# Kernel tuning notes

Measured on AMD Instinct MI355X. Metric: run time of the kernel, lower is better.

The kernel has to match this reference:

```python
import jax, jax.numpy as jnp
import numpy as np

B, S, E, H = 2, 2048, 1024, 16
D = E // H  # head_dim = 64
SCALE = 1.0 / np.sqrt(D)


def setup_inputs() -> dict:
    key = jax.random.key(0)
    ks = jax.random.split(key, 5)
    std = 0.02
    return {
        "x": jax.random.normal(ks[0], (B, S, E), dtype=jnp.float32),
        "wq": jax.random.normal(ks[1], (E, E), dtype=jnp.float32) * std,
        "wk": jax.random.normal(ks[2], (E, E), dtype=jnp.float32) * std,
        "wv": jax.random.normal(ks[3], (E, E), dtype=jnp.float32) * std,
        "wo": jax.random.normal(ks[4], (E, E), dtype=jnp.float32) * std,
    }


def reference(x, wq, wk, wv, wo):
    # Linear projections (torch Linear: y = x @ W.T); weights stored as [out, in]
    q = jnp.einsum('bse,fe->bsf', x, wq)
    k = jnp.einsum('bse,fe->bsf', x, wk)
    v = jnp.einsum('bse,fe->bsf', x, wv)
    # split heads -> [B, H, S, D]
    q = q.reshape(B, S, H, D).transpose(0, 2, 1, 3)
    k = k.reshape(B, S, H, D).transpose(0, 2, 1, 3)
    v = v.reshape(B, S, H, D).transpose(0, 2, 1, 3)
    # scaled dot-product scores [B, H, S, S]
    scores = jnp.einsum('bhqd,bhkd->bhqk', q, k) * SCALE
    # causal mask: -inf above diagonal
    causal = jnp.triu(jnp.full((S, S), -jnp.inf, dtype=scores.dtype), k=1)
    scores = scores + causal[None, None, :, :]
    attn = jax.nn.softmax(scores, axis=-1)
    # dropout p=0 -> identity
    out = jnp.einsum('bhqk,bhkd->bhqd', attn, v)
    out = out.transpose(0, 2, 1, 3).reshape(B, S, E)
    return jnp.einsum('bse,fe->bsf', out, wo)
```

## Files before the change

kernel.cpp:

```cpp
#include <hip/hip_runtime.h>
#include <hip/hip_bf16.h>

#define B_ 2
#define S_ 2048
#define E_ 1024
#define H_ 16
#define D_ 64
#define QKV_N 3072
#define C2_ 0.18033688011112042f

typedef __attribute__((ext_vector_type(8))) unsigned short ushort8_t;
typedef __attribute__((ext_vector_type(8))) short short8_t;
typedef __attribute__((ext_vector_type(4))) float f32x4;

__device__ __forceinline__ unsigned short f2b(float f) {
    union { float f; unsigned u; } x; x.f = f;
    unsigned r = x.u + 0x7FFFu + ((x.u >> 16) & 1u);
    return (unsigned short)(r >> 16);
}
__device__ __forceinline__ ushort2 pkbf(float a, float b) {
    union { __hip_bfloat162 h; ushort2 u; } c;
    c.h = __float22bfloat162_rn(make_float2(a, b));
    return c.u;
}
__device__ __forceinline__ void glds16(const unsigned short* g, unsigned short* l) {
    __builtin_amdgcn_global_load_lds((const __attribute__((address_space(1))) void*)g,
                                     (__attribute__((address_space(3))) void*)l, 16, 0, 0);
}

__global__ __launch_bounds__(256) void cast_all(const float* __restrict__ x,
                                                const float* __restrict__ wq,
                                                const float* __restrict__ wk,
                                                const float* __restrict__ wv,
                                                const float* __restrict__ wo,
                                                unsigned short* __restrict__ xb,
                                                unsigned short* __restrict__ wb) {
    int idx = blockIdx.x * 256 + threadIdx.x;
    const float* src; unsigned short* dst; float s = 1.f; int j;
    if (idx < 1048576) {
        src = x; dst = xb; j = idx;
    } else {
        j = idx - 1048576;
        int y = j >> 18;
        src = (y == 0) ? wq : (y == 1) ? wk : (y == 2) ? wv : wo;
        dst = wb + (size_t)y * 1048576;
        j &= 262143;
        if (y == 0) s = C2_;
    }
    float4 v = ((const float4*)src)[j];
    ushort2 lo = pkbf(v.x * s, v.y * s), hi = pkbf(v.z * s, v.w * s);
    ((ushort4*)dst)[j] = make_ushort4(lo.x, lo.y, hi.x, hi.y);
}

template <int TM, bool OUT_BF16, bool VT>
__device__ __forceinline__ void gemm_bt_body(const unsigned short* __restrict__ A,
                                             const unsigned short* __restrict__ Bt,
                                             void* __restrict__ Cout,
                                             int m0, int n0, int N, int K) {
    __shared__ unsigned short As[2 * TM * 32];
    __shared__ unsigned short Bs[2 * 128 * 32];
    const int tid = threadIdx.x;
    const int wave = tid >> 6;
    const int lane = tid & 63;
    const int wm = (wave >> 1) * (TM / 2);
    const int wn = (wave & 1) * 64;
    const int quad = lane >> 4;
    const int l15 = lane & 15;
    constexpr int MI = TM / 32;

    f32x4 acc[MI][4] = {};

    const int srow = lane >> 2;
    const int scb  = (lane & 3) * 8;
    const unsigned short* gB0 = Bt + (size_t)(n0 + wave * 32 + srow) * K + scb;
    const unsigned short* gB1 = gB0 + (size_t)16 * K;
    unsigned short* lB0 = Bs + wave * 1024;
    unsigned short* lB1 = lB0 + 512;
    const unsigned short* gA0;
    const unsigned short* gA1 = nullptr;
    unsigned short* lA0;
    unsigned short* lA1 = nullptr;
    if (TM == 128) {
        gA0 = A + (size_t)(m0 + wave * 32 + srow) * K + scb;
        gA1 = gA0 + (size_t)16 * K;
        lA0 = As + wave * 1024; lA1 = lA0 + 512;
    } else {
        gA0 = A + (size_t)(m0 + wave * 16 + srow) * K + scb;
        lA0 = As + wave * 512;
    }

    for (int k0 = 0; k0 < K; k0 += 64) {
        __syncthreads();
        glds16(gA0 + k0, lA0);
        glds16(gA0 + k0 + 32, lA0 + TM * 32);
        if (TM == 128) {
            glds16(gA1 + k0, lA1);
            glds16(gA1 + k0 + 32, lA1 + TM * 32);
        }
        glds16(gB0 + k0, lB0);
        glds16(gB0 + k0 + 32, lB0 + 128 * 32);
        glds16(gB1 + k0, lB1);
        glds16(gB1 + k0 + 32, lB1 + 128 * 32);
        __syncthreads();

#pragma unroll
        for (int h = 0; h < 2; ++h) {
            const unsigned short* ah = As + h * TM * 32;
            const unsigned short* bh = Bs + h * 128 * 32;
            short8_t af[MI], bfv[4];
#pragma unroll
            for (int mi = 0; mi < MI; ++mi)
                af[mi] = *(const short8_t*)(&ah[(wm + mi * 16 + l15) * 32 + quad * 8]);
#pragma unroll
            for (int ni = 0; ni < 4; ++ni)
                bfv[ni] = *(const short8_t*)(&bh[(wn + ni * 16 + l15) * 32 + quad * 8]);
#pragma unroll
            for (int mi = 0; mi < MI; ++mi)
#pragma unroll
                for (int ni = 0; ni < 4; ++ni)
                    acc[mi][ni] = __builtin_amdgcn_mfma_f32_16x16x32_bf16(
                        af[mi], bfv[ni], acc[mi][ni], 0, 0, 0);
        }
    }

    if (VT && n0 >= 2048) {
#pragma unroll
        for (int mi = 0; mi < MI; ++mi)
#pragma unroll
            for (int ni = 0; ni < 4; ++ni) {
                int col = n0 + wn + ni * 16 + l15;
                int r0  = m0 + wm + mi * 16 + quad * 4;
                int bb  = r0 >> 11, s = r0 & 2047;
                size_t drow = (size_t)bb * 2048 + 2 * (col - 2048) + (s >> 10);
                unsigned short* dp = (unsigned short*)Cout + drow * QKV_N + 2048 + (s & 1023);
                *(ushort4*)dp = make_ushort4(f2b(acc[mi][ni][0]), f2b(acc[mi][ni][1]),
                                             f2b(acc[mi][ni][2]), f2b(acc[mi][ni][3]));
            }
        return;
    }

#pragma unroll
    for (int mi = 0; mi < MI; ++mi)
#pragma unroll
        for (int ni = 0; ni < 4; ++ni)
#pragma unroll
            for (int r = 0; r < 4; ++r) {
                int row = m0 + wm + mi * 16 + quad * 4 + r;
                int col = n0 + wn + ni * 16 + l15;
                float val = acc[mi][ni][r];
                if (OUT_BF16)
                    ((unsigned short*)Cout)[(size_t)row * N + col] = f2b(val);
                else
                    ((float*)Cout)[(size_t)row * N + col] = val;
            }
}

__global__ __launch_bounds__(256, 3) void gemm_qkv(const unsigned short* __restrict__ xb,
                                                   const unsigned short* __restrict__ wqkv,
                                                   unsigned short* __restrict__ qkv) {
    int id = blockIdx.x + 24 * blockIdx.y;
    int sw = (id & 7) * 96 + (id >> 3);
    int n0 = (sw % 24) * 128;
    int m0 = (sw / 24) * 128;
    gemm_bt_body<128, true, true>(xb, wqkv, qkv, m0, n0, QKV_N, E_);
}

__global__ __launch_bounds__(256, 2) void gemm_out(const unsigned short* __restrict__ a,
                                                   const unsigned short* __restrict__ wob,
                                                   float* __restrict__ c) {
    int id = blockIdx.x + 8 * blockIdx.y;
    int sw = (id & 7) * 64 + (id >> 3);
    gemm_bt_body<64, false, false>(a, wob, c, (sw >> 3) * 64, (sw & 7) * 128, E_, E_);
}

__global__ __launch_bounds__(512, 4) void attn_kernel(const unsigned short* __restrict__ QKV,
                                                      unsigned short* __restrict__ O) {
    __shared__ unsigned short Ks[2][64 * 64];
    __shared__ unsigned short Vs[2][64 * 64];
    __shared__ unsigned short Ps[8][16 * 64];

    const int b = blockIdx.z, h = blockIdx.y;
    const int cx = blockIdx.x;
    const int c0 = (cx & 1) ? (15 - (cx >> 1)) : (cx >> 1);
    const int c = (b == 0) ? c0 : (15 - c0);
    const int tid = threadIdx.x;
    const int w = tid >> 6, lane = tid & 63;
    const int quad = lane >> 4, l15 = lane & 15;
    const int lx = l15 & 7;
    const int chunk = (w < 4) ? (31 - c) : c;
    const int Q0 = chunk * 64 + (w & 3) * 16;

    const size_t qo = (size_t)(b * S_ + Q0 + l15) * QKV_N + h * D_;
    short8_t bq0 = *(const short8_t*)(QKV + qo + quad * 8);
    short8_t bq1 = *(const short8_t*)(QKV + qo + 32 + quad * 8);

    f32x4 Oacc[4] = {};
    f32x4 Lacc = {};
    const int qg = Q0 + l15;
    short8_t ones;
#pragma unroll
    for (int i = 0; i < 8; ++i) ones[i] = (short)0x3F80;

    const int fo0 = ((quad) ^ lx) * 8;
    const int fo1 = ((4 + quad) ^ lx) * 8;
    const int krow = l15 * 64;
    int pwo[4];
#pragma unroll
    for (int tm = 0; tm < 4; ++tm)
        pwo[tm] = ((tm * 2 + (quad >> 1)) ^ lx) * 8 + (quad & 1) * 4;

    const int srow = tid >> 3;
    const int scb  = tid & 7;
    const int swz  = (scb ^ (srow & 7)) * 8;
    const unsigned short* Kbase = QKV + (size_t)(b * S_) * QKV_N + 1024 + h * D_;
    const unsigned short* Vb2 = QKV + (size_t)(b * S_ + 2 * (h * D_ + srow)) * QKV_N + 2048;

    const int ntiles = 32 - c;
    const int nT = (ntiles + 1) >> 1;

    ushort8_t ka = *(const ushort8_t*)(Kbase + (size_t)srow * QKV_N + scb * 8);
    ushort8_t kb = *(const ushort8_t*)(Kbase + (size_t)(64 + srow) * QKV_N + scb * 8);
    ushort8_t va = *(const ushort8_t*)(Vb2 + scb * 8);
    ushort8_t vb = *(const ushort8_t*)(Vb2 + 64 + scb * 8);

    for (int t = 0; t < nT; ++t) {
        const int kt0 = t * 128;
        __syncthreads();
        *(ushort8_t*)(&Ks[0][srow * 64 + swz]) = ka;
        *(ushort8_t*)(&Ks[1][srow * 64 + swz]) = kb;
        *(ushort8_t*)(&Vs[0][srow * 64 + swz]) = va;
        *(ushort8_t*)(&Vs[1][srow * 64 + swz]) = vb;
        __syncthreads();

        if (t + 1 < nT) {
            const int kn = kt0 + 128;
            ka = *(const ushort8_t*)(Kbase + (size_t)(kn + srow) * QKV_N + scb * 8);
            kb = *(const ushort8_t*)(Kbase + (size_t)(kn + 64 + srow) * QKV_N + scb * 8);
            va = *(const ushort8_t*)(Vb2 + (size_t)(kn >> 10) * QKV_N
                                         + (kn & 1023) + scb * 8);
            vb = *(const ushort8_t*)(Vb2 + (size_t)((kn + 64) >> 10) * QKV_N
                                         + ((kn + 64) & 1023) + scb * 8);
        }

#pragma unroll
        for (int s = 0; s < 2; ++s) {
            const int kt = kt0 + s * 64;
            if (kt > Q0 + 15) continue;
            const bool h2 = (kt + 32 <= Q0 + 15);

            if (kt + 63 <= Q0) {
#pragma unroll
                for (int tm = 0; tm < 4; ++tm) {
                    short8_t ak0 = *(const short8_t*)(&Ks[s][tm * 1024 + krow + fo0]);
                    short8_t ak1 = *(const short8_t*)(&Ks[s][tm * 1024 + krow + fo1]);
                    f32x4 st = {0.f, 0.f, 0.f, 0.f};
                    __builtin_amdgcn_s_setprio(1);
                    st = __builtin_amdgcn_mfma_f32_16x16x32_bf16(ak0, bq0, st, 0, 0, 0);
                    st = __builtin_amdgcn_mfma_f32_16x16x32_bf16(ak1, bq1, st, 0, 0, 0);
                    __builtin_amdgcn_s_setprio(0);
                    float p0 = __builtin_amdgcn_exp2f(st[0]);
                    float p1 = __builtin_amdgcn_exp2f(st[1]);
                    float p2 = __builtin_amdgcn_exp2f(st[2]);
                    float p3 = __builtin_amdgcn_exp2f(st[3]);
                    ushort2 a = pkbf(p0, p1), c2 = pkbf(p2, p3);
                    *(ushort4*)(&Ps[w][krow + pwo[tm]]) = make_ushort4(a.x, a.y, c2.x, c2.y);
                }
            } else {
                const int need = h2 ? 4 : 2;
                for (int tm = 0; tm < need; ++tm) {
                    if (kt + tm * 16 <= Q0 + 15) {
                        short8_t ak0 = *(const short8_t*)(&Ks[s][tm * 1024 + krow + fo0]);
                        short8_t ak1 = *(const short8_t*)(&Ks[s][tm * 1024 + krow + fo1]);
                        f32x4 st = {0.f, 0.f, 0.f, 0.f};
                        __builtin_amdgcn_s_setprio(1);
                        st = __builtin_amdgcn_mfma_f32_16x16x32_bf16(ak0, bq0, st, 0, 0, 0);
                        st = __builtin_amdgcn_mfma_f32_16x16x32_bf16(ak1, bq1, st, 0, 0, 0);
                        __builtin_amdgcn_s_setprio(0);
                        const int kvb = kt + tm * 16 + quad * 4;
                        float p0 = (kvb     > qg) ? 0.f : __builtin_amdgcn_exp2f(st[0]);
                        float p1 = (kvb + 1 > qg) ? 0.f : __builtin_amdgcn_exp2f(st[1]);
                        float p2 = (kvb + 2 > qg) ? 0.f : __builtin_amdgcn_exp2f(st[2]);
                        float p3 = (kvb + 3 > qg) ? 0.f : __builtin_amdgcn_exp2f(st[3]);
                        ushort2 a = pkbf(p0, p1), c2 = pkbf(p2, p3);
                        *(ushort4*)(&Ps[w][krow + pwo[tm]]) = make_ushort4(a.x, a.y, c2.x, c2.y);
                    } else {
                        *(ushort4*)(&Ps[w][krow + pwo[tm]]) = make_ushort4(0, 0, 0, 0);
                    }
                }
            }

#pragma unroll
            for (int kh = 0; kh < 2; ++kh) {
                if (kh == 1 && !h2) break;
                const int fo = kh ? fo1 : fo0;
                short8_t bv[4];
#pragma unroll
                for (int tn = 0; tn < 4; ++tn)
                    bv[tn] = *(const short8_t*)(&Vs[s][tn * 1024 + krow + fo]);
                short8_t ap = *(const short8_t*)(&Ps[w][krow + fo]);
                __builtin_amdgcn_s_setprio(1);
#pragma unroll
                for (int tn = 0; tn < 4; ++tn)
                    Oacc[tn] = __builtin_amdgcn_mfma_f32_16x16x32_bf16(
                        ap, bv[tn], Oacc[tn], 0, 0, 0);
                Lacc = __builtin_amdgcn_mfma_f32_16x16x32_bf16(ap, ones, Lacc, 0, 0, 0);
                __builtin_amdgcn_s_setprio(0);
            }
        }
    }

    float lir[4];
#pragma unroll
    for (int r = 0; r < 4; ++r)
        lir[r] = 1.f / Lacc[r];
#pragma unroll
    for (int tn = 0; tn < 4; ++tn)
#pragma unroll
        for (int r = 0; r < 4; ++r) {
            int row = Q0 + quad * 4 + r;
            O[(size_t)(b * S_ + row) * E_ + h * D_ + tn * 16 + l15] =
                f2b(Oacc[tn][r] * lir[r]);
        }
}

extern "C" void kernel_launch(void* const* d_in, const int* in_sizes, int n_in,
                              void* d_out, int out_size, void* d_ws, size_t ws_size,
                              hipStream_t stream) {
    const float* x  = (const float*)d_in[0];
    const float* wq = (const float*)d_in[1];
    const float* wk = (const float*)d_in[2];
    const float* wv = (const float*)d_in[3];
    const float* wo = (const float*)d_in[4];
    float* out = (float*)d_out;

    unsigned short* ws   = (unsigned short*)d_ws;
    unsigned short* xb   = ws;
    unsigned short* wqkv = ws + 4194304;
    unsigned short* wob  = ws + 7340032;
    unsigned short* qkvb = ws + 8388608;
    unsigned short* ab   = ws + 20971520;

    cast_all<<<8192, 256, 0, stream>>>(x, wq, wk, wv, wo, xb, wqkv);
    gemm_qkv<<<dim3(24, 32), 256, 0, stream>>>(xb, wqkv, qkvb);
    attn_kernel<<<dim3(16, 16, 2), 512, 0, stream>>>(qkvb, ab);
    gemm_out<<<dim3(8, 64), 256, 0, stream>>>(ab, wob, out);
}
```

Measured before the change: 162.3 us.

## Rewrite QKV GEMM as dedicated 256x256 tile kernel with swizzled LDS and double buffering

Replaces the generic templated QKV projection GEMM with a dedicated kernel using 256x256 output tiles, 512 threads (8 waves, each computing 128x64), K-step 64, XOR-swizzled LDS layout, and double-buffered direct global-to-LDS loads. It adds s_setprio around the MFMA bursts and barriers between phases. The V-transpose epilogue moves out of the shared body into this kernel. The intent is higher arithmetic intensity and fewer LDS bank conflicts. In exchange it uses 128 KB of LDS per block and only 192 blocks, which may underfill the CUs.

```diff
diff --git a/kernel.cpp b/kernel.cpp
--- a/kernel.cpp
+++ b/kernel.cpp
@@ -123,22 +123,6 @@
         }
     }
 
-    if (VT && n0 >= 2048) {
-#pragma unroll
-        for (int mi = 0; mi < MI; ++mi)
-#pragma unroll
-            for (int ni = 0; ni < 4; ++ni) {
-                int col = n0 + wn + ni * 16 + l15;
-                int r0  = m0 + wm + mi * 16 + quad * 4;
-                int bb  = r0 >> 11, s = r0 & 2047;
-                size_t drow = (size_t)bb * 2048 + 2 * (col - 2048) + (s >> 10);
-                unsigned short* dp = (unsigned short*)Cout + drow * QKV_N + 2048 + (s & 1023);
-                *(ushort4*)dp = make_ushort4(f2b(acc[mi][ni][0]), f2b(acc[mi][ni][1]),
-                                             f2b(acc[mi][ni][2]), f2b(acc[mi][ni][3]));
-            }
-        return;
-    }
-
 #pragma unroll
     for (int mi = 0; mi < MI; ++mi)
 #pragma unroll
@@ -155,14 +139,94 @@
             }
 }
 
-__global__ __launch_bounds__(256, 3) void gemm_qkv(const unsigned short* __restrict__ xb,
-                                                   const unsigned short* __restrict__ wqkv,
-                                                   unsigned short* __restrict__ qkv) {
-    int id = blockIdx.x + 24 * blockIdx.y;
-    int sw = (id & 7) * 96 + (id >> 3);
-    int n0 = (sw % 24) * 128;
-    int m0 = (sw / 24) * 128;
-    gemm_bt_body<128, true, true>(xb, wqkv, qkv, m0, n0, QKV_N, E_);
+__global__ __launch_bounds__(512, 2) void gemm_qkv(const unsigned short* __restrict__ A,
+                                                   const unsigned short* __restrict__ Bt,
+                                                   unsigned short* __restrict__ C) {
+    __shared__ unsigned short As[2][256 * 64];
+    __shared__ unsigned short Bs[2][256 * 64];
+    const int id = blockIdx.x;
+    const int sw = (id & 7) * 24 + (id >> 3);
+    const int m0 = (sw / 12) * 256;
+    const int n0 = (sw % 12) * 256;
+    const int tid = threadIdx.x;
+    const int w = tid >> 6, lane = tid & 63;
+    const int quad = lane >> 4, l15 = lane & 15, lx = l15 & 7;
+    const int wrow = w >> 2, wcol = w & 3;
+
+    f32x4 acc[8][4] = {};
+
+    const int srow = tid >> 3;
+    const int sblk = (tid & 7) ^ (srow & 7);
+    const unsigned short* Asrc = A + (size_t)(m0 + srow) * 1024 + sblk * 8;
+    const unsigned short* Bsrc = Bt + (size_t)(n0 + srow) * 1024 + sblk * 8;
+    const int dofs = w * 512;
+
+    auto stage = [&](int slot, int k) {
+#pragma unroll
+        for (int rb = 0; rb < 4; ++rb)
+            glds16(Asrc + (size_t)rb * 64 * 1024 + k * 64, &As[slot][rb * 4096 + dofs]);
+#pragma unroll
+        for (int rb = 0; rb < 4; ++rb)
+            glds16(Bsrc + (size_t)rb * 64 * 1024 + k * 64, &Bs[slot][rb * 4096 + dofs]);
+    };
+
+    stage(0, 0);
+    __syncthreads();
+
+    for (int t = 0; t < 16; ++t) {
+        if (t + 1 < 16) stage((t + 1) & 1, t + 1);
+        const unsigned short* a   = As[t & 1];
+        const unsigned short* bsh = Bs[t & 1];
+#pragma unroll
+        for (int ph = 0; ph < 4; ++ph) {
+            const int kh  = ph >> 1;
+            const int mih = (ph & 1) * 4;
+            const int fo  = ((quad + 4 * kh) ^ lx) * 8;
+            short8_t af[4], bf[4];
+#pragma unroll
+            for (int i = 0; i < 4; ++i)
+                af[i] = *(const short8_t*)(&a[(wrow * 128 + (mih + i) * 16 + l15) * 64 + fo]);
+#pragma unroll
+            for (int ni = 0; ni < 4; ++ni)
+                bf[ni] = *(const short8_t*)(&bsh[(wcol * 64 + ni * 16 + l15) * 64 + fo]);
+            __builtin_amdgcn_s_setprio(1);
+#pragma unroll
+            for (int i = 0; i < 4; ++i)
+#pragma unroll
+                for (int ni = 0; ni < 4; ++ni)
+                    acc[mih + i][ni] = __builtin_amdgcn_mfma_f32_16x16x32_bf16(
+                        af[i], bf[ni], acc[mih + i][ni], 0, 0, 0);
+            __builtin_amdgcn_s_setprio(0);
+            if (ph < 3) __builtin_amdgcn_s_barrier();
+        }
+        __syncthreads();
+    }
+
+    if (n0 >= 2048) {
+#pragma unroll
+        for (int mi = 0; mi < 8; ++mi)
+#pragma unroll
+            for (int ni = 0; ni < 4; ++ni) {
+                int col = n0 + wcol * 64 + ni * 16 + l15;
+                int r0  = m0 + wrow * 128 + mi * 16 + quad * 4;
+                int bb  = r0 >> 11, s = r0 & 2047;
+                size_t drow = (size_t)bb * 2048 + 2 * (col - 2048) + (s >> 10);
+                unsigned short* dp = C + drow * QKV_N + 2048 + (s & 1023);
+                *(ushort4*)dp = make_ushort4(f2b(acc[mi][ni][0]), f2b(acc[mi][ni][1]),
+                                             f2b(acc[mi][ni][2]), f2b(acc[mi][ni][3]));
+            }
+    } else {
+#pragma unroll
+        for (int mi = 0; mi < 8; ++mi)
+#pragma unroll
+            for (int ni = 0; ni < 4; ++ni)
+#pragma unroll
+                for (int r = 0; r < 4; ++r) {
+                    int row = m0 + wrow * 128 + mi * 16 + quad * 4 + r;
+                    int col = n0 + wcol * 64 + ni * 16 + l15;
+                    C[(size_t)row * QKV_N + col] = f2b(acc[mi][ni][r]);
+                }
+    }
 }
 
 __global__ __launch_bounds__(256, 2) void gemm_out(const unsigned short* __restrict__ a,
@@ -341,7 +405,7 @@
     unsigned short* ab   = ws + 20971520;
 
     cast_all<<<8192, 256, 0, stream>>>(x, wq, wk, wv, wo, xb, wqkv);
-    gemm_qkv<<<dim3(24, 32), 256, 0, stream>>>(xb, wqkv, qkvb);
+    gemm_qkv<<<192, 512, 0, stream>>>(xb, wqkv, qkvb);
     attn_kernel<<<dim3(16, 16, 2), 512, 0, stream>>>(qkvb, ab);
     gemm_out<<<dim3(8, 64), 256, 0, stream>>>(ab, wob, out);
 }
```

Result: slower. 176.7 us (+8.9%).
